# Kernel tuning notes

Hardware: AMD Instinct MI355X
Metric: run time of the kernel (lower is better)

Reference implementation:

```python
import jax, jax.numpy as jnp
import numpy as np

B, D, TOPC = 8, 1024, 256
CIN, DOWN, BR, NR, G = 64, 128, 2, 8, 8
GC = DOWN // G
H = W = 64
LN_EPS = 1e-5


def _ln(x, g, b):
    mu = x.mean(-1, keepdims=True)
    var = ((x - mu) ** 2).mean(-1, keepdims=True)
    return (x - mu) * jax.lax.rsqrt(var + LN_EPS) * g + b


def _gelu(x):
    return jax.nn.gelu(x, approximate=False)


def _sample_topleft(I, IX, IY, IT, x, y):
    # x, y: [B, N] continuous coords; returns [B, CIN, N]
    x = x[:, None, :]
    y = y[:, None, :]
    X = jnp.ceil(x).astype(jnp.int32)
    Y = jnp.ceil(y).astype(jnp.int32)
    z = jnp.zeros_like(X)
    dx = X - x
    dy = Y - y
    b = jnp.arange(B)[:, None, None]
    c = jnp.arange(CIN)[None, :, None]
    wx1 = 0.5 * dx ** 2
    wx2 = dx - wx1
    wy1 = 0.5 * dy ** 2
    wy2 = dy - wy1
    s_a = IT[b, c, X, Y]
    s_e1 = (wy1 * (IX[b, c, X, Y - 1] - 0.5 * I[b, c, X, Y - 1] - 0.5 * I[b, c, z, Y - 1])
            + wy2 * (IX[b, c, X, Y] - 0.5 * I[b, c, X, Y] - 0.5 * I[b, c, z, Y]))
    s_e2 = (wx1 * (IY[b, c, X - 1, Y] - 0.5 * I[b, c, X - 1, Y] - 0.5 * I[b, c, X - 1, z])
            + wx2 * (IY[b, c, X, Y] - 0.5 * I[b, c, X, Y] - 0.5 * I[b, c, X, z]))
    s_c = (wx1 * wy1 * I[b, c, X - 1, Y - 1] + wx2 * wy1 * I[b, c, X, Y - 1]
           + wx1 * wy2 * I[b, c, X - 1, Y] + wx2 * wy2 * I[b, c, X, Y])
    return s_a - s_e1 - s_e2 + s_c


def setup_inputs() -> dict:
    key = jax.random.key(0)
    ks = jax.random.split(key, 20)
    s = 0.02
    return {
        "x": jax.random.normal(ks[0], (B, D, TOPC), jnp.float32),
        "I": jax.random.normal(ks[1], (B, CIN, H, W), jnp.float32),
        "IX": jax.random.normal(ks[2], (B, CIN, H, W), jnp.float32),
        "IY": jax.random.normal(ks[3], (B, CIN, H, W), jnp.float32),
        "IT": jax.random.normal(ks[4], (B, CIN, H, W), jnp.float32),
        "w_idx": jax.random.normal(ks[5], (BR * NR * 4, TOPC), jnp.float32) * s,
        "b_idx": jnp.zeros((BR * NR * 4,), jnp.float32),
        "w_proj": jax.random.normal(ks[6], (DOWN, CIN), jnp.float32) * s,
        "b_proj": jnp.zeros((DOWN,), jnp.float32),
        "w_mask": jax.random.normal(ks[7], (BR * NR * G, TOPC), jnp.float32) * s,
        "b_mask": jnp.zeros((BR * NR * G,), jnp.float32),
        "g1": jnp.ones((DOWN,), jnp.float32),
        "beta1": jnp.zeros((DOWN,), jnp.float32),
        "w_mlp1": jax.random.normal(ks[8], (4 * DOWN, DOWN), jnp.float32) * s,
        "b_mlp1": jnp.zeros((4 * DOWN,), jnp.float32),
        "w_mlp2": jax.random.normal(ks[9], (DOWN, 4 * DOWN), jnp.float32) * s,
        "b_mlp2": jnp.zeros((DOWN,), jnp.float32),
        "g2": jnp.ones((DOWN,), jnp.float32),
        "beta2": jnp.zeros((DOWN,), jnp.float32),
    }


def reference(x, I, IX, IY, IT, w_idx, b_idx, w_proj, b_proj, w_mask, b_mask,
              g1, beta1, w_mlp1, b_mlp1, w_mlp2, b_mlp2, g2, beta2):
    # rect prediction
    p = x @ w_idx.T + b_idx                       # [B, D, BR*NR*4]
    fac = jnp.array([H - 1, W - 1, H - 1, W - 1], jnp.float32)
    p = jax.nn.sigmoid(p.reshape(B, D, BR, NR, 4)) * fac
    p = p.reshape(B, D * BR * NR, 4)
    x1, y1, x2, y2 = p[:, :, 0], p[:, :, 1], p[:, :, 2], p[:, :, 3]
    S = (_sample_topleft(I, IX, IY, IT, x2, y2)
         - _sample_topleft(I, IX, IY, IT, x1, y2)
         - _sample_topleft(I, IX, IY, IT, x2, y1)
         + _sample_topleft(I, IX, IY, IT, x1, y1))  # [B, CIN, N]
    S = S.reshape(B, CIN, D, BR, NR).transpose(0, 2, 3, 4, 1)  # [B, D, BR, NR, CIN]
    rects = _gelu(S @ w_proj.T + b_proj)           # [B, D, BR, NR, DOWN]
    mask = (x @ w_mask.T + b_mask).reshape(B, D * BR, NR, G, 1)
    mask = jax.nn.softmax(mask, axis=2)
    rects = rects.reshape(B, D * BR, NR, G, GC)
    out = (mask * rects).sum(2).reshape(B, D * BR, DOWN)
    out = _ln(out, g1, beta1)
    shortcut = out
    out = _gelu(out @ w_mlp1.T + b_mlp1) @ w_mlp2.T + b_mlp2
    return _ln(out, g2, beta2) + shortcut
```

## Files before the change

### kernel.cpp

```cpp
#include <hip/hip_runtime.h>
#include <hip/hip_bf16.h>
#include <hip/hip_fp16.h>
#include <math.h>

#define BB   8
#define DD   1024

typedef short bh8 __attribute__((ext_vector_type(8)));
typedef float f32x4 __attribute__((ext_vector_type(4)));
typedef _Float16 h2f __attribute__((ext_vector_type(2)));

__device__ __forceinline__ ushort f2bf(float f) {
    uint u = __builtin_bit_cast(uint, f);
    u += 0x7fffu + ((u >> 16) & 1u);
    return (ushort)(u >> 16);
}
__device__ __forceinline__ float asf(uint u)  { return __builtin_bit_cast(float, u); }
__device__ __forceinline__ uint  pkh(float a, float b) {
    return __builtin_bit_cast(uint, __builtin_amdgcn_cvt_pkrtz(a, b));
}
__device__ __forceinline__ h2f ash2f(uint u) { return __builtin_bit_cast(h2f, u); }

#if __has_builtin(__builtin_amdgcn_fdot2)
__device__ __forceinline__ float fdot2h(h2f a, h2f b, float c) {
    return __builtin_amdgcn_fdot2(a, b, c, false);
}
#else
__device__ __forceinline__ float fdot2h(h2f a, h2f b, float c) {
    return fmaf((float)a.x, (float)b.x, fmaf((float)a.y, (float)b.y, c));
}
#endif

__device__ __forceinline__ uint cvtpk_bf16(float a, float b) {
    uint r;
    asm("v_cvt_pk_bf16_f32 %0, %1, %2" : "=v"(r) : "v"(a), "v"(b));
    return r;
}
__device__ __forceinline__ ushort cvt1_bf16(float a) {
    uint r;
    asm("v_cvt_pk_bf16_f32 %0, %1, %2" : "=v"(r) : "v"(a), "v"(a));
    return (ushort)r;
}

__device__ __forceinline__ float gelu_fast(float x) {
    float x2 = x * x;
#if __has_builtin(__builtin_amdgcn_exp2f)
    float e = __builtin_amdgcn_exp2f(x * fmaf(x2, -0.20588652f, -2.3022082f));
#else
    float e = __expf(-(1.5957691216f * x + 0.14270963f * x * x2));
#endif
    return x * __builtin_amdgcn_rcpf(1.0f + e);
}
__device__ __forceinline__ float sig63(float v) {
    return 63.0f * __builtin_amdgcn_rcpf(1.0f + __expf(-v));
}

__global__ __launch_bounds__(256) void kT_cat(
    const float* __restrict__ w_idx, const float* __restrict__ w_mask,
    float* __restrict__ w_catT)
{
    int e = blockIdx.x * 256 + threadIdx.x;
    int k = e / 192, o = e - k * 192;
    const float* src = (o < 64) ? (w_idx + (size_t)o * 256)
                                : (w_mask + (size_t)(o - 64) * 256);
    w_catT[e] = src[k];
}

__global__ __launch_bounds__(256) void k01(
    const float* __restrict__ x, const float* __restrict__ w_catT,
    const float* __restrict__ b_idx, const float* __restrict__ b_mask,
    float* __restrict__ maskw, uint* __restrict__ meta,
    const float* __restrict__ I, const float* __restrict__ IX,
    const float* __restrict__ IY, const float* __restrict__ IT,
    uint4* __restrict__ T1, ushort* __restrict__ T2,
    const float* __restrict__ w_proj, const float* __restrict__ w1,
    const float* __restrict__ w2,
    ushort* __restrict__ w_projP, ushort* __restrict__ w1P,
    ushort* __restrict__ w2P)
{
    __shared__ __align__(16) char smem[24960];
    int t = threadIdx.x;
    int bid = blockIdx.x;

    if (bid < 1024) {
        float (*xs)[256]   = (float (*)[256])(smem);
        float (*sOut)[192] = (float (*)[192])(smem + 8192);
        size_t rowbase = (size_t)bid * 8;

        for (int i = t; i < 2048; i += 256) xs[i >> 8][i & 255] = x[rowbase * 256 + i];
        __syncthreads();

        if (t < 192) {
            float acc[8] = {0.f, 0.f, 0.f, 0.f, 0.f, 0.f, 0.f, 0.f};
            #pragma unroll 4
            for (int k = 0; k < 256; ++k) {
                float wv = w_catT[k * 192 + t];
                #pragma unroll
                for (int r = 0; r < 8; ++r) acc[r] += xs[r][k] * wv;
            }
            #pragma unroll
            for (int r = 0; r < 8; ++r) sOut[r][t] = acc[r];
        }
        __syncthreads();

        if (t < 128) {
            int row = t >> 4, u = t & 15, br = u >> 3, nr = u & 7;
            int c0 = br * 32 + nr * 4;
            float x1 = sig63(sOut[row][c0 + 0] + b_idx[c0 + 0]);
            float y1 = sig63(sOut[row][c0 + 1] + b_idx[c0 + 1]);
            float x2 = sig63(sOut[row][c0 + 2] + b_idx[c0 + 2]);
            float y2 = sig63(sOut[row][c0 + 3] + b_idx[c0 + 3]);
            int X1 = (int)ceilf(x1); X1 = X1 < 1 ? 1 : (X1 > 63 ? 63 : X1);
            int X2 = (int)ceilf(x2); X2 = X2 < 1 ? 1 : (X2 > 63 ? 63 : X2);
            int Y1 = (int)ceilf(y1); Y1 = Y1 < 1 ? 1 : (Y1 > 63 ? 63 : Y1);
            int Y2 = (int)ceilf(y2); Y2 = Y2 < 1 ? 1 : (Y2 > 63 ? 63 : Y2);
            float dxa = (float)X1 - x1, dxb = (float)X2 - x2;
            float dya = (float)Y1 - y1, dyb = (float)Y2 - y2;
            int   Xc[4] = {X2, X1, X2, X1};
            int   Yc[4] = {Y2, Y2, Y1, Y1};
            float sg[4] = {1.f, -1.f, -1.f, 1.f};
            float dxc[4] = {dxb, dxa, dxb, dxa};
            float dyc[4] = {dyb, dyb, dya, dya};
            uint* mr = meta + (((rowbase + row) * 16) + (size_t)u) * 32;
            #pragma unroll
            for (int c = 0; c < 4; ++c) {
                uint pt = (uint)(Xc[c] * 64 + Yc[c]);
                float s = sg[c], dx = dxc[c], dy = dyc[c];
                float dx2 = dx * dx, dy2 = dy * dy;
                uint4 wa, wb;
                wa.x = pt * 1024u;
                wa.y = pt * 128u;
                wa.z = pkh(s, s * dy);
                wa.w = pkh(s * dy2, s * dx);
                wb.x = pkh(s * dx2, s * dx * dy);
                wb.y = pkh(s * dx * dy2, s * dx2 * dy);
                wb.z = __builtin_bit_cast(uint, s * dx2 * dy2);
                wb.w = 0u;
                *(uint4*)(mr + c * 8 + 0) = wa;
                *(uint4*)(mr + c * 8 + 4) = wb;
            }
        } else {
            int tt = t - 128;
            int row = tt >> 4, br = (tt >> 3) & 1, g = tt & 7;
            float lg[8];
            float mx = -1e30f;
            #pragma unroll
            for (int nr = 0; nr < 8; ++nr) {
                int idx = br * 64 + nr * 8 + g;
                lg[nr] = sOut[row][64 + idx] + b_mask[idx];
                mx = fmaxf(mx, lg[nr]);
            }
            float s = 0.f;
            #pragma unroll
            for (int nr = 0; nr < 8; ++nr) { lg[nr] = __expf(lg[nr] - mx); s += lg[nr]; }
            float inv = __builtin_amdgcn_rcpf(s);
            #pragma unroll
            for (int nr = 0; nr < 8; ++nr)
                maskw[(rowbase + row) * 128 + br * 64 + nr * 8 + g] = lg[nr] * inv;
        }
    } else if (bid < 3072) {
        float (*tI)[65]  = (float (*)[65])(smem);
        float (*tIp)[65] = (float (*)[65])(smem + 4160);
        float (*tX)[65]  = (float (*)[65])(smem + 8320);
        float (*tY)[65]  = (float (*)[65])(smem + 12480);
        float (*tYp)[65] = (float (*)[65])(smem + 16640);
        float (*tT)[65]  = (float (*)[65])(smem + 20800);
        int kb = bid - 1024;
        int chunk = kb & 3, h = (kb >> 2) & 63, b = kb >> 8;
        int hp = h > 0 ? h - 1 : 0;
        int cb = chunk * 16;
        size_t inb  = (size_t)b * 262144 + (size_t)h  * 64;
        size_t inbp = (size_t)b * 262144 + (size_t)hp * 64;

        #pragma unroll
        for (int i = 0; i < 4; ++i) {
            int idx = i * 256 + t; int c = idx >> 6, w = idx & 63;
            size_t o = (size_t)(cb + c) * 4096 + w;
            tI[c][w]  = I[inb + o];
            tIp[c][w] = I[inbp + o];
            tX[c][w]  = IX[inb + o];
            tY[c][w]  = IY[inb + o];
            tYp[c][w] = IY[inbp + o];
            tT[c][w]  = IT[inb + o];
        }
        __syncthreads();

        #pragma unroll
        for (int i = 0; i < 4; ++i) {
            int idx = i * 256 + t; int w = idx >> 4, c = idx & 15;
            int wm = w > 0 ? w - 1 : 0;
            float I00 = tI[c][w], I0m = tI[c][wm];
            float Im0 = tIp[c][w], Imm = tIp[c][wm];
            float E1  = tX[c][w]  - 0.5f * I00;
            float E1m = tX[c][wm] - 0.5f * I0m;
            float E2  = tY[c][w]  - 0.5f * I00;
            float E2m = tYp[c][w] - 0.5f * Im0;
            float v0 = tT[c][w];
            float v1 = -E1;
            float v2 = 0.5f * (E1 - E1m);
            float v3 = -E2;
            float v4 = 0.5f * (E2 - E2m);
            float v5 = I00;
            float v6 = 0.5f * (I0m - I00);
            float v7 = 0.5f * (Im0 - I00);
            float v8 = 0.25f * ((Imm - I0m) - (Im0 - I00));
            size_t pt = (((size_t)b * 4096) + (size_t)h * 64 + w) * 64 + (cb + c);
            uint4 o4;
            o4.x = pkh(v0, v1);
            o4.y = pkh(v2, v3);
            o4.z = pkh(v4, v5);
            o4.w = pkh(v6, v7);
            T1[pt] = o4;
            T2[pt] = (ushort)(pkh(v8, 0.f) & 0xffffu);
        }
    } else {
        int e = (bid - 3072 + 192) * 256 + t;
        if (e < 50176) {
            int g = e - 49152; int nt = g >> 7, ks = (g >> 6) & 1, l = g & 63;
            int n = nt * 16 + (l & 15), k0 = ks * 32 + (l >> 4) * 8;
            ushort* dst = w_projP + (size_t)g * 8;
            #pragma unroll
            for (int j = 0; j < 8; ++j) dst[j] = f2bf(w_proj[n * 64 + k0 + j]);
        } else if (e < 58368) {
            int g = e - 50176; int nt = g >> 8, ks = (g >> 6) & 3, l = g & 63;
            int n = nt * 16 + (l & 15), k0 = ks * 32 + (l >> 4) * 8;
            ushort* dst = w1P + (size_t)g * 8;
            #pragma unroll
            for (int j = 0; j < 8; ++j) dst[j] = f2bf(w1[n * 128 + k0 + j]);
        } else if (e < 66560) {
            int g = e - 58368; int nt = g >> 10, ks = (g >> 6) & 15, l = g & 63;
            int n = nt * 16 + (l & 15), k0 = ks * 32 + (l >> 4) * 8;
            ushort* dst = w2P + (size_t)g * 8;
            #pragma unroll
            for (int j = 0; j < 8; ++j) dst[j] = f2bf(w2[n * 512 + k0 + j]);
        }
    }
}

__global__ __launch_bounds__(256) void k2_rects(
    const uint4* __restrict__ T1, const ushort* __restrict__ T2,
    const uint* __restrict__ meta,
    const ushort* __restrict__ w_projP, const float* __restrict__ b_proj,
    const float* __restrict__ maskw, const float* __restrict__ g1,
    const float* __restrict__ beta1, float* __restrict__ mid)
{
    __shared__ __align__(16) uint meta_lds[16][32];
    __shared__ __align__(16) float S_lds[16][68];
    __shared__ float mrow[128];
    __shared__ float outr[2][128];
    int bid = blockIdx.x;
    int b = bid & 7, d = bid >> 3;
    int t = threadIdx.x, w = t >> 6, l = t & 63;
    size_t tile = (size_t)b * DD + d;
    if (t < 128) {
        uint4 mv = *(const uint4*)(meta + tile * 512 + (size_t)t * 4);
        *(uint4*)(&meta_lds[0][0] + t * 4) = mv;
    }
    if (t >= 128) mrow[t - 128] = maskw[tile * 128 + (t - 128)];

    bh8 bf[2][2];
    #pragma unroll
    for (int ni = 0; ni < 2; ++ni) {
        int nt = w * 2 + ni;
        #pragma unroll
        for (int ks = 0; ks < 2; ++ks)
            bf[ni][ks] = *(const bh8*)(w_projP + ((size_t)(nt * 2 + ks) * 64 + l) * 8);
    }
    __syncthreads();
    const char* t1b = ((const char*)T1) + ((size_t)b << 22) + (size_t)(l * 16);
    const char* t2b = ((const char*)T2) + ((size_t)b << 19) + (size_t)(l * 2);

    uint4 q[4]; ushort e8[4];
    {
        int m0 = w * 4;
        #pragma unroll
        for (int c = 0; c < 4; ++c) {
            q[c]  = *(const uint4*)(t1b + meta_lds[m0][c * 8 + 0]);
            e8[c] = *(const ushort*)(t2b + meta_lds[m0][c * 8 + 1]);
        }
    }
    #pragma unroll
    for (int rr = 0; rr < 4; ++rr) {
        int m = w * 4 + rr;
        uint4 qc[4]; ushort ec[4];
        #pragma unroll
        for (int c = 0; c < 4; ++c) { qc[c] = q[c]; ec[c] = e8[c]; }
        if (rr < 3) {
            int mn = m + 1;
            #pragma unroll
            for (int c = 0; c < 4; ++c) {
                q[c]  = *(const uint4*)(t1b + meta_lds[mn][c * 8 + 0]);
                e8[c] = *(const ushort*)(t2b + meta_lds[mn][c * 8 + 1]);
            }
        }
        float acc0 = 0.f, acc1 = 0.f;
        #pragma unroll
        for (int c = 0; c < 4; ++c) {
            uint cz = meta_lds[m][c * 8 + 2], cw = meta_lds[m][c * 8 + 3];
            uint bx = meta_lds[m][c * 8 + 4], by = meta_lds[m][c * 8 + 5];
            float bz = asf(meta_lds[m][c * 8 + 6]);
            float ev = __half2float(__builtin_bit_cast(__half, ec[c]));
            float cv = bz * ev;
            cv = fdot2h(ash2f(by), ash2f(qc[c].w), cv);
            cv = fdot2h(ash2f(bx), ash2f(qc[c].z), cv);
            cv = fdot2h(ash2f(cw), ash2f(qc[c].y), cv);
            cv = fdot2h(ash2f(cz), ash2f(qc[c].x), cv);
            if (c & 1) acc1 += cv; else acc0 += cv;
        }
        S_lds[m][l] = acc0 + acc1;
    }
    __syncthreads();

    int am = l & 15, q2 = l >> 4;
    bh8 a0, a1;
    {
        float4 va = *(const float4*)&S_lds[am][q2 * 8];
        float4 vb = *(const float4*)&S_lds[am][q2 * 8 + 4];
        uint4 ua;
        ua.x = cvtpk_bf16(va.x, va.y);
        ua.y = cvtpk_bf16(va.z, va.w);
        ua.z = cvtpk_bf16(vb.x, vb.y);
        ua.w = cvtpk_bf16(vb.z, vb.w);
        a0 = __builtin_bit_cast(bh8, ua);
        float4 vc = *(const float4*)&S_lds[am][32 + q2 * 8];
        float4 vd = *(const float4*)&S_lds[am][32 + q2 * 8 + 4];
        uint4 ub;
        ub.x = cvtpk_bf16(vc.x, vc.y);
        ub.y = cvtpk_bf16(vc.z, vc.w);
        ub.z = cvtpk_bf16(vd.x, vd.y);
        ub.w = cvtpk_bf16(vd.z, vd.w);
        a1 = __builtin_bit_cast(bh8, ub);
    }
    f32x4 cc[2];
    cc[0] = (f32x4){0.f, 0.f, 0.f, 0.f};
    cc[1] = (f32x4){0.f, 0.f, 0.f, 0.f};
    cc[0] = __builtin_amdgcn_mfma_f32_16x16x32_bf16(a0, bf[0][0], cc[0], 0, 0, 0);
    cc[0] = __builtin_amdgcn_mfma_f32_16x16x32_bf16(a1, bf[0][1], cc[0], 0, 0, 0);
    cc[1] = __builtin_amdgcn_mfma_f32_16x16x32_bf16(a0, bf[1][0], cc[1], 0, 0, 0);
    cc[1] = __builtin_amdgcn_mfma_f32_16x16x32_bf16(a1, bf[1][1], cc[1], 0, 0, 0);

    int cl = l & 15;
    #pragma unroll
    for (int ni = 0; ni < 2; ++ni) {
        int nt = w * 2 + ni;
        int col = nt * 16 + cl;
        float bpv = b_proj[col];
        float p = 0.f;
        #pragma unroll
        for (int reg = 0; reg < 4; ++reg) {
            int r = q2 * 4 + reg;
            float v = cc[ni][reg] + bpv;
            p += gelu_fast(v) * mrow[(r >> 3) * 64 + (r & 7) * 8 + nt];
        }
        p += __shfl_xor(p, 16, 64);
        if (q2 == 0) outr[0][col] = p;
        else if (q2 == 2) outr[1][col] = p;
    }
    __syncthreads();

    if (w < 2) {
        float v0 = outr[w][l], v1 = outr[w][l + 64];
        float s = v0 + v1, sq = v0 * v0 + v1 * v1;
        #pragma unroll
        for (int mm = 32; mm > 0; mm >>= 1) {
            s  += __shfl_xor(s, mm, 64);
            sq += __shfl_xor(sq, mm, 64);
        }
        float mu  = s * (1.0f / 128.0f);
        float var = sq * (1.0f / 128.0f) - mu * mu;
        float rs  = rsqrtf(var + 1e-5f);
        size_t ob = (tile * 2 + w) * 128;
        mid[ob + l]      = (v0 - mu) * rs * g1[l]      + beta1[l];
        mid[ob + l + 64] = (v1 - mu) * rs * g1[l + 64] + beta1[l + 64];
    }
}

__global__ __launch_bounds__(256) void k4_mlp(
    const float* __restrict__ mid, const ushort* __restrict__ w1P,
    const float* __restrict__ b1, const ushort* __restrict__ w2P,
    const float* __restrict__ b2, const float* __restrict__ g2,
    const float* __restrict__ beta2, float* __restrict__ outp)
{
    __shared__ float xr[16][132];
    __shared__ __align__(16) ushort Af[4][64][8];
    __shared__ __align__(16) ushort H[16][520];
    __shared__ float oo[16][128];
    __shared__ float b1s[512];
    __shared__ float b2s[128], g2s[128], bt2s[128];
    int t = threadIdx.x, w = t >> 6, l = t & 63;
    int bid = blockIdx.x;
    int mt = (bid & 7) * 128 + (bid >> 3);
    size_t rowbase = (size_t)mt * 16;

    for (int i = t; i < 2048; i += 256) xr[i >> 7][i & 127] = mid[rowbase * 128 + i];
    for (int i = t; i < 512; i += 256) b1s[i] = b1[i];
    if (t < 128) { b2s[t] = b2[t]; g2s[t] = g2[t]; bt2s[t] = beta2[t]; }
    __syncthreads();

    {
        int ks = t >> 6, m = l & 15, c0 = ks * 32 + (l >> 4) * 8;
        uint* dst = (uint*)&Af[ks][l][0];
        #pragma unroll
        for (int j = 0; j < 4; ++j)
            dst[j] = cvtpk_bf16(xr[m][c0 + 2 * j], xr[m][c0 + 2 * j + 1]);
    }
    __syncthreads();

    f32x4 c1[8];
    #pragma unroll
    for (int i = 0; i < 8; ++i) c1[i] = (f32x4){0.f, 0.f, 0.f, 0.f};
    bh8 a[4];
    #pragma unroll
    for (int ks = 0; ks < 4; ++ks) a[ks] = *(const bh8*)&Af[ks][l][0];
    #pragma unroll
    for (int ni = 0; ni < 8; ++ni) {
        int nt = w * 8 + ni;
        #pragma unroll
        for (int ks = 0; ks < 4; ++ks) {
            bh8 bfr = *(const bh8*)(w1P + ((size_t)(nt * 4 + ks) * 64 + l) * 8);
            c1[ni] = __builtin_amdgcn_mfma_f32_16x16x32_bf16(a[ks], bfr, c1[ni], 0, 0, 0);
        }
    }
    #pragma unroll
    for (int ni = 0; ni < 8; ++ni) {
        int nt = w * 8 + ni;
        int col = nt * 16 + (l & 15);
        int r0 = (l >> 4) * 4;
        #pragma unroll
        for (int reg = 0; reg < 4; ++reg)
            H[r0 + reg][col] = cvt1_bf16(gelu_fast(c1[ni][reg] + b1s[col]));
    }
    __syncthreads();

    f32x4 c2[2];
    c2[0] = (f32x4){0.f, 0.f, 0.f, 0.f};
    c2[1] = (f32x4){0.f, 0.f, 0.f, 0.f};
    const char* hb = (const char*)&H[0][0];
    #pragma unroll
    for (int ks2 = 0; ks2 < 16; ++ks2) {
        bh8 af = *(const bh8*)(hb + (l & 15) * 1040 + ks2 * 64 + (l >> 4) * 16);
        #pragma unroll
        for (int i = 0; i < 2; ++i) {
            int nt2 = w * 2 + i;
            bh8 bfr = *(const bh8*)(w2P + ((size_t)(nt2 * 16 + ks2) * 64 + l) * 8);
            c2[i] = __builtin_amdgcn_mfma_f32_16x16x32_bf16(af, bfr, c2[i], 0, 0, 0);
        }
    }
    #pragma unroll
    for (int i = 0; i < 2; ++i) {
        int col = (w * 2 + i) * 16 + (l & 15);
        int r0 = (l >> 4) * 4;
        #pragma unroll
        for (int reg = 0; reg < 4; ++reg) oo[r0 + reg][col] = c2[i][reg] + b2s[col];
    }
    __syncthreads();

    #pragma unroll
    for (int rr = 0; rr < 4; ++rr) {
        int r = w * 4 + rr;
        float v0 = oo[r][l], v1 = oo[r][l + 64];
        float s = v0 + v1, sq = v0 * v0 + v1 * v1;
        #pragma unroll
        for (int m = 32; m > 0; m >>= 1) {
            s  += __shfl_xor(s, m, 64);
            sq += __shfl_xor(sq, m, 64);
        }
        float mu  = s * (1.0f / 128.0f);
        float var = sq * (1.0f / 128.0f) - mu * mu;
        float rs  = rsqrtf(var + 1e-5f);
        size_t ob = (rowbase + r) * 128;
        outp[ob + l]      = (v0 - mu) * rs * g2s[l]      + bt2s[l]      + xr[r][l];
        outp[ob + l + 64] = (v1 - mu) * rs * g2s[l + 64] + bt2s[l + 64] + xr[r][l + 64];
    }
}

extern "C" void kernel_launch(void* const* d_in, const int* in_sizes, int n_in,
                              void* d_out, int out_size, void* d_ws, size_t ws_size,
                              hipStream_t stream) {
    const float* x      = (const float*)d_in[0];
    const float* I      = (const float*)d_in[1];
    const float* IX     = (const float*)d_in[2];
    const float* IY     = (const float*)d_in[3];
    const float* IT     = (const float*)d_in[4];
    const float* w_idx  = (const float*)d_in[5];
    const float* b_idx  = (const float*)d_in[6];
    const float* w_proj = (const float*)d_in[7];
    const float* b_proj = (const float*)d_in[8];
    const float* w_mask = (const float*)d_in[9];
    const float* b_mask = (const float*)d_in[10];
    const float* g1     = (const float*)d_in[11];
    const float* beta1  = (const float*)d_in[12];
    const float* w_mlp1 = (const float*)d_in[13];
    const float* b_mlp1 = (const float*)d_in[14];
    const float* w_mlp2 = (const float*)d_in[15];
    const float* b_mlp2 = (const float*)d_in[16];
    const float* g2     = (const float*)d_in[17];
    const float* beta2  = (const float*)d_in[18];
    float* out = (float*)d_out;

    float* ws = (float*)d_ws;
    float*  w_catT  = ws;
    ushort* w_projP = (ushort*)(ws + 49152);
    ushort* w1P     = (ushort*)(ws + 53248);
    ushort* w2P     = (ushort*)(ws + 86016);
    float*  maskw   = ws + 118784;
    uint*   meta    = (uint*)(ws + 1167360);
    uint4*  T1      = (uint4*)(ws + 5361664);
    ushort* T2      = (ushort*)(ws + 13750272);

    kT_cat<<<192, 256, 0, stream>>>(w_idx, w_mask, w_catT);
    k01<<<3140, 256, 0, stream>>>(x, w_catT, b_idx, b_mask, maskw, meta,
                                  I, IX, IY, IT, T1, T2,
                                  w_proj, w_mlp1, w_mlp2,
                                  w_projP, w1P, w2P);
    k2_rects<<<8192, 256, 0, stream>>>(T1, T2, meta, w_projP, b_proj, maskw,
                                       g1, beta1, out);
    k4_mlp<<<1024, 256, 0, stream>>>(out, w1P, b_mlp1, w2P, b_mlp2, g2, beta2, out);
}
```

Baseline: 96.38 us.

## Vectorize table staging, drop x LDS staging, deepen gather prefetch

The projection GEMM in k01 now reads x directly from global memory (relying on the cache) instead of staging it in LDS, and loads eight weight rows at a time. The table-building blocks stage their input planes with float4 loads into a single padded float array. The sampling kernel double-buffers its gathers two rows ahead and uses readfirstlane on uniform offsets so addressing can use scalar registers. The aim is fewer load instructions and more latency hiding, at the cost of higher register pressure and uncached-looking broadcast x reads.

After: 107.7 us. 1.12x slower.

```diff
diff --git a/kernel.cpp b/kernel.cpp
--- a/kernel.cpp
+++ b/kernel.cpp
@@ -78,25 +78,28 @@
     ushort* __restrict__ w_projP, ushort* __restrict__ w1P,
     ushort* __restrict__ w2P)
 {
-    __shared__ __align__(16) char smem[24960];
+    __shared__ __align__(16) float sf[6528];
     int t = threadIdx.x;
     int bid = blockIdx.x;
 
     if (bid < 1024) {
-        float (*xs)[256]   = (float (*)[256])(smem);
-        float (*sOut)[192] = (float (*)[192])(smem + 8192);
+        float (*sOut)[192] = (float (*)[192])sf;
         size_t rowbase = (size_t)bid * 8;
-
-        for (int i = t; i < 2048; i += 256) xs[i >> 8][i & 255] = x[rowbase * 256 + i];
-        __syncthreads();
+        const float* xp = x + rowbase * 256;
 
         if (t < 192) {
             float acc[8] = {0.f, 0.f, 0.f, 0.f, 0.f, 0.f, 0.f, 0.f};
-            #pragma unroll 4
-            for (int k = 0; k < 256; ++k) {
-                float wv = w_catT[k * 192 + t];
+            for (int k0c = 0; k0c < 256; k0c += 8) {
+                float wv[8];
                 #pragma unroll
-                for (int r = 0; r < 8; ++r) acc[r] += xs[r][k] * wv;
+                for (int kk = 0; kk < 8; ++kk)
+                    wv[kk] = w_catT[(k0c + kk) * 192 + t];
+                #pragma unroll
+                for (int r = 0; r < 8; ++r) {
+                    #pragma unroll
+                    for (int kk = 0; kk < 8; ++kk)
+                        acc[r] = fmaf(xp[r * 256 + k0c + kk], wv[kk], acc[r]);
+                }
             }
             #pragma unroll
             for (int r = 0; r < 8; ++r) sOut[r][t] = acc[r];
@@ -159,12 +162,6 @@
                 maskw[(rowbase + row) * 128 + br * 64 + nr * 8 + g] = lg[nr] * inv;
         }
     } else if (bid < 3072) {
-        float (*tI)[65]  = (float (*)[65])(smem);
-        float (*tIp)[65] = (float (*)[65])(smem + 4160);
-        float (*tX)[65]  = (float (*)[65])(smem + 8320);
-        float (*tY)[65]  = (float (*)[65])(smem + 12480);
-        float (*tYp)[65] = (float (*)[65])(smem + 16640);
-        float (*tT)[65]  = (float (*)[65])(smem + 20800);
         int kb = bid - 1024;
         int chunk = kb & 3, h = (kb >> 2) & 63, b = kb >> 8;
         int hp = h > 0 ? h - 1 : 0;
@@ -172,16 +169,16 @@
         size_t inb  = (size_t)b * 262144 + (size_t)h  * 64;
         size_t inbp = (size_t)b * 262144 + (size_t)hp * 64;
 
-        #pragma unroll
-        for (int i = 0; i < 4; ++i) {
-            int idx = i * 256 + t; int c = idx >> 6, w = idx & 63;
-            size_t o = (size_t)(cb + c) * 4096 + w;
-            tI[c][w]  = I[inb + o];
-            tIp[c][w] = I[inbp + o];
-            tX[c][w]  = IX[inb + o];
-            tY[c][w]  = IY[inb + o];
-            tYp[c][w] = IY[inbp + o];
-            tT[c][w]  = IT[inb + o];
+        {
+            int c = t >> 4, w4 = (t & 15) << 2;
+            size_t o = (size_t)(cb + c) * 4096 + w4;
+            int so = c * 68 + w4;
+            *(float4*)(sf + 0 * 1088 + so) = *(const float4*)(I  + inb  + o);
+            *(float4*)(sf + 1 * 1088 + so) = *(const float4*)(I  + inbp + o);
+            *(float4*)(sf + 2 * 1088 + so) = *(const float4*)(IX + inb  + o);
+            *(float4*)(sf + 3 * 1088 + so) = *(const float4*)(IY + inb  + o);
+            *(float4*)(sf + 4 * 1088 + so) = *(const float4*)(IY + inbp + o);
+            *(float4*)(sf + 5 * 1088 + so) = *(const float4*)(IT + inb  + o);
         }
         __syncthreads();
 
@@ -189,13 +186,14 @@
         for (int i = 0; i < 4; ++i) {
             int idx = i * 256 + t; int w = idx >> 4, c = idx & 15;
             int wm = w > 0 ? w - 1 : 0;
-            float I00 = tI[c][w], I0m = tI[c][wm];
-            float Im0 = tIp[c][w], Imm = tIp[c][wm];
-            float E1  = tX[c][w]  - 0.5f * I00;
-            float E1m = tX[c][wm] - 0.5f * I0m;
-            float E2  = tY[c][w]  - 0.5f * I00;
-            float E2m = tYp[c][w] - 0.5f * Im0;
-            float v0 = tT[c][w];
+            int rb = c * 68;
+            float I00 = sf[rb + w],        I0m = sf[rb + wm];
+            float Im0 = sf[1088 + rb + w], Imm = sf[1088 + rb + wm];
+            float E1  = sf[2176 + rb + w]  - 0.5f * I00;
+            float E1m = sf[2176 + rb + wm] - 0.5f * I0m;
+            float E2  = sf[3264 + rb + w]  - 0.5f * I00;
+            float E2m = sf[4352 + rb + w]  - 0.5f * Im0;
+            float v0 = sf[5440 + rb + w];
             float v1 = -E1;
             float v2 = 0.5f * (E1 - E1m);
             float v3 = -E2;
@@ -270,27 +268,33 @@
     const char* t1b = ((const char*)T1) + ((size_t)b << 22) + (size_t)(l * 16);
     const char* t2b = ((const char*)T2) + ((size_t)b << 19) + (size_t)(l * 2);
 
-    uint4 q[4]; ushort e8[4];
-    {
-        int m0 = w * 4;
+    int m0 = w * 4;
+    uint4 q[2][4]; ushort e8[2][4];
+    #pragma unroll
+    for (int g = 0; g < 2; ++g) {
         #pragma unroll
         for (int c = 0; c < 4; ++c) {
-            q[c]  = *(const uint4*)(t1b + meta_lds[m0][c * 8 + 0]);
-            e8[c] = *(const ushort*)(t2b + meta_lds[m0][c * 8 + 1]);
+            uint o1 = __builtin_amdgcn_readfirstlane(meta_lds[m0 + g][c * 8 + 0]);
+            uint o2 = __builtin_amdgcn_readfirstlane(meta_lds[m0 + g][c * 8 + 1]);
+            q[g][c]  = *(const uint4*)(t1b + o1);
+            e8[g][c] = *(const ushort*)(t2b + o2);
         }
     }
     #pragma unroll
     for (int rr = 0; rr < 4; ++rr) {
-        int m = w * 4 + rr;
+        int m = m0 + rr;
+        int cur = rr & 1;
         uint4 qc[4]; ushort ec[4];
         #pragma unroll
-        for (int c = 0; c < 4; ++c) { qc[c] = q[c]; ec[c] = e8[c]; }
-        if (rr < 3) {
-            int mn = m + 1;
+        for (int c = 0; c < 4; ++c) { qc[c] = q[cur][c]; ec[c] = e8[cur][c]; }
+        if (rr < 2) {
+            int mn = m + 2;
             #pragma unroll
             for (int c = 0; c < 4; ++c) {
-                q[c]  = *(const uint4*)(t1b + meta_lds[mn][c * 8 + 0]);
-                e8[c] = *(const ushort*)(t2b + meta_lds[mn][c * 8 + 1]);
+                uint o1 = __builtin_amdgcn_readfirstlane(meta_lds[mn][c * 8 + 0]);
+                uint o2 = __builtin_amdgcn_readfirstlane(meta_lds[mn][c * 8 + 1]);
+                q[cur][c]  = *(const uint4*)(t1b + o1);
+                e8[cur][c] = *(const ushort*)(t2b + o2);
             }
         }
         float acc0 = 0.f, acc1 = 0.f;
```
